# Kernel tuning notes

Measured on AMD Instinct MI355X. Metric: run time of the kernel, lower is better.

The kernel has to match this reference:

```python
import jax, jax.numpy as jnp
import numpy as np

N, E = 50000, 800000
IN_DIM, H, D = 128, 8, 16  # num_heads=8, out_dim(per head)=16


def setup_inputs() -> dict:
    key = jax.random.key(0)
    ks = jax.random.split(key, 9)
    s = 1.0 / np.sqrt(IN_DIM)
    return {
        "h": jax.random.normal(ks[0], (N, IN_DIM), dtype=jnp.float32),
        "Wq": jax.random.normal(ks[1], (IN_DIM, H * D), dtype=jnp.float32) * s,
        "bq": jnp.zeros((H * D,), dtype=jnp.float32),
        "Wk": jax.random.normal(ks[2], (IN_DIM, H * D), dtype=jnp.float32) * s,
        "bk": jnp.zeros((H * D,), dtype=jnp.float32),
        "Wv": jax.random.normal(ks[3], (IN_DIM, H * D), dtype=jnp.float32) * s,
        "bv": jnp.zeros((H * D,), dtype=jnp.float32),
        "src": jax.random.randint(ks[4], (E,), 0, N, dtype=jnp.int32),
        "dst": jax.random.randint(ks[5], (E,), 0, N, dtype=jnp.int32),
    }


def reference(h, Wq, bq, Wk, bk, Wv, bv, src, dst):
    n = h.shape[0]
    Q = (h @ Wq + bq).reshape(n, H, D)
    K = (h @ Wk + bk).reshape(n, H, D)
    V = (h @ Wv + bv).reshape(n, H, D)
    # edge score: u_mul_v(K, Q).sum(-1) / sqrt(D), clamped to [-5, 5]
    score = jnp.einsum("ehd,ehd->eh", K[src], Q[dst]) / jnp.sqrt(
        jnp.asarray(D, h.dtype)
    )  # [E, H]
    score = jnp.clip(score, -5.0, 5.0)
    # edge_softmax over edges sharing the same destination node
    smax = jax.ops.segment_max(score, dst, num_segments=n)  # [N, H]
    ex = jnp.exp(score - smax[dst])
    denom = jax.ops.segment_sum(ex, dst, num_segments=n)  # [N, H]
    a = ex / denom[dst]  # [E, H]
    # u_mul_e(V, a) then sum to destination
    m = V[src] * a[:, :, None]  # [E, H, D]
    wV = jax.ops.segment_sum(m, dst, num_segments=n)  # [N, H, D]
    return wV.reshape(n, H * D)
```

## Files before the change

kernel.cpp:

```cpp
#include <hip/hip_runtime.h>
#include <hip/hip_bf16.h>


typedef short short8 __attribute__((ext_vector_type(8)));
typedef float f32x4 __attribute__((ext_vector_type(4)));

__device__ __forceinline__ unsigned pack_bf16(float a, float b) {
    unsigned ua = __float_as_uint(a), ub = __float_as_uint(b);
    ua += 0x7fffu + ((ua >> 16) & 1u);
    ub += 0x7fffu + ((ub >> 16) & 1u);
    return (ua >> 16) | (ub & 0xffff0000u);
}

#define ULO(u) __uint_as_float((u) << 16)
#define UHI(u) __uint_as_float((u) & 0xffff0000u)

__global__ __launch_bounds__(256) void prep_all(
    const float* __restrict__ W0, const float* __restrict__ W1,
    const float* __restrict__ W2, unsigned char* __restrict__ WTb,
    int* __restrict__ counts, int n)
{
    const int b = blockIdx.x;
    if (b < 24) {
        const int w   = b >> 3;
        const int idx = (b & 7) * 256 + threadIdx.x;
        const float* W = (w == 0) ? W0 : (w == 1) ? W1 : W2;
        unsigned char* wt = WTb + w * 32768;
        const int kp = idx >> 5;
        const int c4 = (idx & 31) * 4;
        const float* Wp = W + (size_t)(2 * kp) * 128 + c4;
        float4 wa = *(const float4*)Wp;
        float4 wb = *(const float4*)(Wp + 128);
        float a0[4] = {wa.x, wa.y, wa.z, wa.w};
        float a1[4] = {wb.x, wb.y, wb.z, wb.w};
#pragma unroll
        for (int i = 0; i < 4; ++i) {
            const int col = c4 + i;
            *(unsigned*)(wt + col * 256 + ((4 * kp) ^ ((col & 7) << 4))) =
                pack_bf16(a0[i], a1[i]);
        }
    } else {
        const int i = (b - 24) * 256 + threadIdx.x;
        if (i < n) counts[i] = 0;
    }
}

__global__ void hist_rank(const int* __restrict__ dst, int* __restrict__ counts,
                          int* __restrict__ rank, int e) {
    int i = blockIdx.x * blockDim.x + threadIdx.x;
    if (i < e) rank[i] = atomicAdd(&counts[dst[i]], 1);
}

__global__ void scan_block_sums(const int* __restrict__ counts, int* __restrict__ bsums, int nelem) {
    __shared__ int red[4];
    int i = blockIdx.x * 256 + threadIdx.x;
    int v = (i < nelem) ? counts[i] : 0;
#pragma unroll
    for (int o = 32; o > 0; o >>= 1) v += __shfl_down(v, o, 64);
    if ((threadIdx.x & 63) == 0) red[threadIdx.x >> 6] = v;
    __syncthreads();
    if (threadIdx.x == 0) bsums[blockIdx.x] = red[0] + red[1] + red[2] + red[3];
}

__global__ void scan_final2(const int* __restrict__ counts, const int* __restrict__ bsums,
                            int* __restrict__ offsets, int nelem, int e) {
    __shared__ int tmp[256];
    __shared__ int red[4];
    const int t = threadIdx.x;

    int pre = (t < blockIdx.x) ? bsums[t] : 0;
#pragma unroll
    for (int o = 32; o > 0; o >>= 1) pre += __shfl_down(pre, o, 64);
    if ((t & 63) == 0) red[t >> 6] = pre;
    __syncthreads();
    const int base = red[0] + red[1] + red[2] + red[3];

    const int i = blockIdx.x * 256 + t;
    int v = (i < nelem) ? counts[i] : 0;
    tmp[t] = v;
    __syncthreads();
    for (int o = 1; o < 256; o <<= 1) {
        int u = (t >= o) ? tmp[t - o] : 0;
        __syncthreads();
        tmp[t] += u;
        __syncthreads();
    }
    if (i < nelem) offsets[i] = base + tmp[t] - v;
    if (i == nelem) offsets[nelem] = e;
}

__global__ void fill_kernel(const int* __restrict__ src, const int* __restrict__ dst,
                            const int* __restrict__ rank, const int* __restrict__ offsets,
                            int* __restrict__ srcSorted, int e) {
    int i = blockIdx.x * blockDim.x + threadIdx.x;
    if (i < e) srcSorted[offsets[dst[i]] + rank[i]] = src[i];
}

__global__ __launch_bounds__(512) void qkv_gemm(
    const float* __restrict__ h, const unsigned char* __restrict__ WTb,
    const float* __restrict__ b0, const float* __restrict__ b1,
    const float* __restrict__ b2,
    unsigned* __restrict__ qb, unsigned* __restrict__ kb, unsigned* __restrict__ vb,
    int n)
{
    __shared__ __align__(16) unsigned char lds[32768];
    const int tid  = threadIdx.x;
    const int row0 = blockIdx.x * 64;

    for (int idx = tid; idx < 2048; idx += 512) {
        const int row = idx >> 5;
        const int c4  = (idx & 31) * 4;
        float4 v = make_float4(0.f, 0.f, 0.f, 0.f);
        if (row0 + row < n) v = *(const float4*)(h + (size_t)(row0 + row) * 128 + c4);
        *(uint2*)(lds + row * 256 + ((c4 * 2) ^ ((row & 7) << 4))) =
            make_uint2(pack_bf16(v.x, v.y), pack_bf16(v.z, v.w));
    }

    const float* bs[3] = {b0, b1, b2};
    unsigned* planes[3] = {qb, kb, vb};

    const int lane = tid & 63, wave = tid >> 6;
    const int wr = wave >> 2, wc = wave & 3;
    const int lr = lane & 15, lg = lane >> 4;

    __syncthreads();

    short8 af[2][4];
#pragma unroll
    for (int mt = 0; mt < 2; ++mt)
#pragma unroll
        for (int ks = 0; ks < 4; ++ks) {
            const int row = wr * 32 + mt * 16 + lr;
            const int kbyte = ks * 64 + lg * 16;
            af[mt][ks] = *(const short8*)(lds + row * 256 + (kbyte ^ ((row & 7) << 4)));
        }

    for (int w = 0; w < 3; ++w) {
        short8 bf[2][4];
#pragma unroll
        for (int nt = 0; nt < 2; ++nt)
#pragma unroll
            for (int ks = 0; ks < 4; ++ks) {
                const int col = wc * 32 + nt * 16 + lr;
                const int kbyte = ks * 64 + lg * 16;
                bf[nt][ks] = *(const short8*)(
                    WTb + w * 32768 + col * 256 + (kbyte ^ ((col & 7) << 4)));
            }

        f32x4 acc[2][2];
#pragma unroll
        for (int nt = 0; nt < 2; ++nt) {
            const float bv = bs[w][wc * 32 + nt * 16 + lr];
            acc[0][nt] = (f32x4){bv, bv, bv, bv};
            acc[1][nt] = (f32x4){bv, bv, bv, bv};
        }
#pragma unroll
        for (int ks = 0; ks < 4; ++ks)
#pragma unroll
            for (int mt = 0; mt < 2; ++mt)
#pragma unroll
                for (int nt = 0; nt < 2; ++nt)
                    acc[mt][nt] = __builtin_amdgcn_mfma_f32_16x16x32_bf16(
                        af[mt][ks], bf[nt][ks], acc[mt][nt], 0, 0, 0);

        __syncthreads();
        {
            unsigned* epi = (unsigned*)(lds + 16384);
#pragma unroll
            for (int mt = 0; mt < 2; ++mt)
#pragma unroll
                for (int nt = 0; nt < 2; ++nt) {
                    const int col = wc * 32 + nt * 16 + lr;
#pragma unroll
                    for (int r = 0; r < 4; ++r) {
                        const int row = wr * 32 + mt * 16 + lg * 4 + r;
                        const float v  = acc[mt][nt][r];
                        const float vn = __shfl_xor(v, 1);
                        if (!(lane & 1)) epi[row * 64 + (col >> 1)] = pack_bf16(v, vn);
                    }
                }
        }
        __syncthreads();
        {
            const uint4* s = (const uint4*)(lds + 16384);
            uint4* d = (uint4*)(planes[w] + (size_t)row0 * 64);
            d[tid]       = s[tid];
            d[tid + 512] = s[tid + 512];
        }
    }
}

__global__ __launch_bounds__(256) void mha_node(
    const unsigned* __restrict__ Qb, const unsigned* __restrict__ Kb,
    const unsigned* __restrict__ Vb,
    const int* __restrict__ offsets, const int* __restrict__ srcSorted,
    float* __restrict__ out, int n)
{
    const int lane = threadIdx.x & 63;
    const int node = (blockIdx.x * blockDim.x + threadIdx.x) >> 6;
    if (node >= n) return;

    const unsigned qu = Qb[(size_t)node * 64 + lane];
    const float qx = ULO(qu) * 0.25f, qy = UHI(qu) * 0.25f;
    const int beg = offsets[node], end = offsets[node + 1];

    float accx = 0.f, accy = 0.f, lsum = 0.f;

#define EDGE_COMPUTE(ku, vu)                                          \
    {                                                                 \
        float prod = fmaf(ULO(ku), qx, UHI(ku) * qy);                 \
        prod += __shfl_xor(prod, 1);                                  \
        prod += __shfl_xor(prod, 2);                                  \
        prod += __shfl_xor(prod, 4);                                  \
        float sc = fminf(5.f, fmaxf(-5.f, prod));                     \
        float p = __expf(sc);                                         \
        lsum += p;                                                    \
        accx = fmaf(p, ULO(vu), accx);                                \
        accy = fmaf(p, UHI(vu), accy);                                \
    }

    for (int j0 = beg; j0 < end; j0 += 64) {
        const int rem = end - j0;
        const int cnt = rem < 64 ? rem : 64;
        int myS = (lane < cnt) ? srcSorted[j0 + lane] : 0;

        int t = 0;
        for (; t + 8 <= cnt; t += 8) {
            unsigned ku[8], vu[8];
#pragma unroll
            for (int u = 0; u < 8; ++u) {
                int s = __shfl(myS, t + u);
                ku[u] = Kb[(size_t)s * 64 + lane];
                vu[u] = Vb[(size_t)s * 64 + lane];
            }
#pragma unroll
            for (int u = 0; u < 8; ++u) EDGE_COMPUTE(ku[u], vu[u]);
        }
        for (; t < cnt; ++t) {
            int s = __shfl(myS, t);
            unsigned ku0 = Kb[(size_t)s * 64 + lane];
            unsigned vu0 = Vb[(size_t)s * 64 + lane];
            EDGE_COMPUTE(ku0, vu0);
        }
    }

    float inv = (lsum > 0.f) ? 1.f / lsum : 0.f;
    *(float2*)(out + (size_t)node * 128 + lane * 2) =
        make_float2(accx * inv, accy * inv);
}

extern "C" void kernel_launch(void* const* d_in, const int* in_sizes, int n_in,
                              void* d_out, int out_size, void* d_ws, size_t ws_size,
                              hipStream_t stream) {
    const float* h  = (const float*)d_in[0];
    const float* Wq = (const float*)d_in[1];
    const float* bq = (const float*)d_in[2];
    const float* Wk = (const float*)d_in[3];
    const float* bk = (const float*)d_in[4];
    const float* Wv = (const float*)d_in[5];
    const float* bv = (const float*)d_in[6];
    const int*   src = (const int*)d_in[7];
    const int*   dst = (const int*)d_in[8];
    float* out = (float*)d_out;

    const int n = in_sizes[0] / 128;
    const int e = in_sizes[7];
    const int nblk = (n + 63) / 64;
    const int npad = nblk * 64;
    const int nb = (n + 255) / 256;

    char* ws = (char*)d_ws;
    size_t off = 0;
    auto alloc = [&](size_t bytes) {
        char* p = ws + off;
        off = (off + bytes + 255) & ~(size_t)255;
        return p;
    };
    unsigned char* WTb = (unsigned char*)alloc(3 * 32768);
    unsigned* Qb       = (unsigned*)alloc((size_t)npad * 64 * 4);
    unsigned* Kb       = (unsigned*)alloc((size_t)npad * 64 * 4);
    unsigned* Vb       = (unsigned*)alloc((size_t)npad * 64 * 4);
    int* counts        = (int*)alloc((size_t)n * sizeof(int));
    int* offsets       = (int*)alloc((size_t)(n + 1) * sizeof(int));
    int* rank          = (int*)alloc((size_t)e * sizeof(int));
    int* bsums         = (int*)alloc((size_t)nb * sizeof(int));
    int* srcSorted     = (int*)alloc((size_t)e * sizeof(int));
    (void)ws_size; (void)n_in; (void)out_size;

    prep_all<<<24 + nb, 256, 0, stream>>>(Wq, Wk, Wv, WTb, counts, n);
    hist_rank<<<(e + 255) / 256, 256, 0, stream>>>(dst, counts, rank, e);
    scan_block_sums<<<nb, 256, 0, stream>>>(counts, bsums, n);
    scan_final2<<<nb, 256, 0, stream>>>(counts, bsums, offsets, n, e);
    fill_kernel<<<(e + 255) / 256, 256, 0, stream>>>(src, dst, rank, offsets, srcSorted, e);
    qkv_gemm<<<nblk, 512, 0, stream>>>(h, WTb, bq, bk, bv, Qb, Kb, Vb, n);
    mha_node<<<((size_t)n * 64 + 255) / 256, 256, 0, stream>>>(
        Qb, Kb, Vb, offsets, srcSorted, out, n);
}
```

Before: 143.7 us.

## Interleave K and V per node and compute transposed GEMM without LDS

K and V projections are now written into one interleaved buffer, so each edge gather in the attention kernel fetches K and V with a single 8-byte load per lane instead of two separate 4-byte loads from different planes. The QKV GEMM is transposed: weights become the A operand and h rows are loaded straight from global into registers as the B operand. This removes the LDS staging, the swizzle, and the block barriers. Outputs are written directly from the accumulators, which makes the stores less coalesced (scattered 4-byte writes for K and V) in exchange for better gather locality in the dominant edge loop.

After: 162.6 us. +13.2%, slower.

```diff
diff --git a/kernel.cpp b/kernel.cpp
--- a/kernel.cpp
+++ b/kernel.cpp
@@ -36,8 +36,7 @@
 #pragma unroll
         for (int i = 0; i < 4; ++i) {
             const int col = c4 + i;
-            *(unsigned*)(wt + col * 256 + ((4 * kp) ^ ((col & 7) << 4))) =
-                pack_bf16(a0[i], a1[i]);
+            *(unsigned*)(wt + col * 256 + kp * 4) = pack_bf16(a0[i], a1[i]);
         }
     } else {
         const int i = (b - 24) * 256 + threadIdx.x;
@@ -96,64 +95,56 @@
     if (i < e) srcSorted[offsets[dst[i]] + rank[i]] = src[i];
 }
 
-__global__ __launch_bounds__(512) void qkv_gemm(
+__global__ __launch_bounds__(512) void qkv_gemm_t(
     const float* __restrict__ h, const unsigned char* __restrict__ WTb,
     const float* __restrict__ b0, const float* __restrict__ b1,
     const float* __restrict__ b2,
-    unsigned* __restrict__ qb, unsigned* __restrict__ kb, unsigned* __restrict__ vb,
-    int n)
+    unsigned* __restrict__ qb, unsigned* __restrict__ kvb, int n)
 {
-    __shared__ __align__(16) unsigned char lds[32768];
     const int tid  = threadIdx.x;
+    const int lane = tid & 63, wave = tid >> 6;
+    const int a = wave >> 2;
+    const int bq4 = wave & 3;
+    const int lr = lane & 15, lg = lane >> 4;
     const int row0 = blockIdx.x * 64;
 
-    for (int idx = tid; idx < 2048; idx += 512) {
-        const int row = idx >> 5;
-        const int c4  = (idx & 31) * 4;
-        float4 v = make_float4(0.f, 0.f, 0.f, 0.f);
-        if (row0 + row < n) v = *(const float4*)(h + (size_t)(row0 + row) * 128 + c4);
-        *(uint2*)(lds + row * 256 + ((c4 * 2) ^ ((row & 7) << 4))) =
-            make_uint2(pack_bf16(v.x, v.y), pack_bf16(v.z, v.w));
+    short8 hf[2][4];
+#pragma unroll
+    for (int nt = 0; nt < 2; ++nt) {
+        const int node = row0 + a * 32 + nt * 16 + lr;
+        const bool ok = node < n;
+        const float* hp = h + (size_t)node * 128;
+#pragma unroll
+        for (int ks = 0; ks < 4; ++ks) {
+            const int k0 = ks * 32 + lg * 8;
+            float4 x = ok ? *(const float4*)(hp + k0)     : make_float4(0.f,0.f,0.f,0.f);
+            float4 y = ok ? *(const float4*)(hp + k0 + 4) : make_float4(0.f,0.f,0.f,0.f);
+            uint4 u = make_uint4(pack_bf16(x.x, x.y), pack_bf16(x.z, x.w),
+                                 pack_bf16(y.x, y.y), pack_bf16(y.z, y.w));
+            hf[nt][ks] = *(short8*)&u;
+        }
     }
 
     const float* bs[3] = {b0, b1, b2};
-    unsigned* planes[3] = {qb, kb, vb};
-
-    const int lane = tid & 63, wave = tid >> 6;
-    const int wr = wave >> 2, wc = wave & 3;
-    const int lr = lane & 15, lg = lane >> 4;
-
-    __syncthreads();
-
-    short8 af[2][4];
-#pragma unroll
-    for (int mt = 0; mt < 2; ++mt)
-#pragma unroll
-        for (int ks = 0; ks < 4; ++ks) {
-            const int row = wr * 32 + mt * 16 + lr;
-            const int kbyte = ks * 64 + lg * 16;
-            af[mt][ks] = *(const short8*)(lds + row * 256 + (kbyte ^ ((row & 7) << 4)));
-        }
 
     for (int w = 0; w < 3; ++w) {
-        short8 bf[2][4];
-#pragma unroll
-        for (int nt = 0; nt < 2; ++nt)
-#pragma unroll
-            for (int ks = 0; ks < 4; ++ks) {
-                const int col = wc * 32 + nt * 16 + lr;
-                const int kbyte = ks * 64 + lg * 16;
-                bf[nt][ks] = *(const short8*)(
-                    WTb + w * 32768 + col * 256 + (kbyte ^ ((col & 7) << 4)));
-            }
+        short8 af[2][4];
+#pragma unroll
+        for (int mt = 0; mt < 2; ++mt) {
+            const unsigned char* wp = WTb + w * 32768 + (bq4 * 32 + mt * 16 + lr) * 256;
+#pragma unroll
+            for (int ks = 0; ks < 4; ++ks)
+                af[mt][ks] = *(const short8*)(wp + ks * 64 + lg * 16);
+        }
 
         f32x4 acc[2][2];
 #pragma unroll
-        for (int nt = 0; nt < 2; ++nt) {
-            const float bv = bs[w][wc * 32 + nt * 16 + lr];
-            acc[0][nt] = (f32x4){bv, bv, bv, bv};
-            acc[1][nt] = (f32x4){bv, bv, bv, bv};
-        }
+        for (int mt = 0; mt < 2; ++mt) {
+            const float4 bv = *(const float4*)(bs[w] + bq4 * 32 + mt * 16 + lg * 4);
+            acc[mt][0] = (f32x4){bv.x, bv.y, bv.z, bv.w};
+            acc[mt][1] = acc[mt][0];
+        }
+
 #pragma unroll
         for (int ks = 0; ks < 4; ++ks)
 #pragma unroll
@@ -161,38 +152,32 @@
 #pragma unroll
                 for (int nt = 0; nt < 2; ++nt)
                     acc[mt][nt] = __builtin_amdgcn_mfma_f32_16x16x32_bf16(
-                        af[mt][ks], bf[nt][ks], acc[mt][nt], 0, 0, 0);
-
-        __syncthreads();
-        {
-            unsigned* epi = (unsigned*)(lds + 16384);
-#pragma unroll
-            for (int mt = 0; mt < 2; ++mt)
-#pragma unroll
-                for (int nt = 0; nt < 2; ++nt) {
-                    const int col = wc * 32 + nt * 16 + lr;
-#pragma unroll
-                    for (int r = 0; r < 4; ++r) {
-                        const int row = wr * 32 + mt * 16 + lg * 4 + r;
-                        const float v  = acc[mt][nt][r];
-                        const float vn = __shfl_xor(v, 1);
-                        if (!(lane & 1)) epi[row * 64 + (col >> 1)] = pack_bf16(v, vn);
-                    }
+                        af[mt][ks], hf[nt][ks], acc[mt][nt], 0, 0, 0);
+
+#pragma unroll
+        for (int mt = 0; mt < 2; ++mt) {
+            const int pi = bq4 * 16 + mt * 8 + lg * 2;
+#pragma unroll
+            for (int nt = 0; nt < 2; ++nt) {
+                const int node = row0 + a * 32 + nt * 16 + lr;
+                const unsigned u0 = pack_bf16(acc[mt][nt][0], acc[mt][nt][1]);
+                const unsigned u1 = pack_bf16(acc[mt][nt][2], acc[mt][nt][3]);
+                if (w == 0) {
+                    *(uint2*)(qb + (size_t)node * 64 + pi) = make_uint2(u0, u1);
+                } else if (w == 1) {
+                    kvb[(size_t)node * 128 + 2 * pi]     = u0;
+                    kvb[(size_t)node * 128 + 2 * pi + 2] = u1;
+                } else {
+                    kvb[(size_t)node * 128 + 2 * pi + 1] = u0;
+                    kvb[(size_t)node * 128 + 2 * pi + 3] = u1;
                 }
-        }
-        __syncthreads();
-        {
-            const uint4* s = (const uint4*)(lds + 16384);
-            uint4* d = (uint4*)(planes[w] + (size_t)row0 * 64);
-            d[tid]       = s[tid];
-            d[tid + 512] = s[tid + 512];
+            }
         }
     }
 }
 
 __global__ __launch_bounds__(256) void mha_node(
-    const unsigned* __restrict__ Qb, const unsigned* __restrict__ Kb,
-    const unsigned* __restrict__ Vb,
+    const unsigned* __restrict__ Qb, const uint2* __restrict__ KV,
     const int* __restrict__ offsets, const int* __restrict__ srcSorted,
     float* __restrict__ out, int n)
 {
@@ -206,17 +191,17 @@
 
     float accx = 0.f, accy = 0.f, lsum = 0.f;
 
-#define EDGE_COMPUTE(ku, vu)                                          \
+#define EDGE_COMPUTE(kv)                                              \
     {                                                                 \
-        float prod = fmaf(ULO(ku), qx, UHI(ku) * qy);                 \
+        float prod = fmaf(ULO((kv).x), qx, UHI((kv).x) * qy);         \
         prod += __shfl_xor(prod, 1);                                  \
         prod += __shfl_xor(prod, 2);                                  \
         prod += __shfl_xor(prod, 4);                                  \
         float sc = fminf(5.f, fmaxf(-5.f, prod));                     \
         float p = __expf(sc);                                         \
         lsum += p;                                                    \
-        accx = fmaf(p, ULO(vu), accx);                                \
-        accy = fmaf(p, UHI(vu), accy);                                \
+        accx = fmaf(p, ULO((kv).y), accx);                            \
+        accy = fmaf(p, UHI((kv).y), accy);                            \
     }
 
     for (int j0 = beg; j0 < end; j0 += 64) {
@@ -226,21 +211,19 @@
 
         int t = 0;
         for (; t + 8 <= cnt; t += 8) {
-            unsigned ku[8], vu[8];
+            uint2 kv[8];
 #pragma unroll
             for (int u = 0; u < 8; ++u) {
                 int s = __shfl(myS, t + u);
-                ku[u] = Kb[(size_t)s * 64 + lane];
-                vu[u] = Vb[(size_t)s * 64 + lane];
+                kv[u] = KV[(size_t)s * 64 + lane];
             }
 #pragma unroll
-            for (int u = 0; u < 8; ++u) EDGE_COMPUTE(ku[u], vu[u]);
+            for (int u = 0; u < 8; ++u) EDGE_COMPUTE(kv[u]);
         }
         for (; t < cnt; ++t) {
             int s = __shfl(myS, t);
-            unsigned ku0 = Kb[(size_t)s * 64 + lane];
-            unsigned vu0 = Vb[(size_t)s * 64 + lane];
-            EDGE_COMPUTE(ku0, vu0);
+            uint2 kv0 = KV[(size_t)s * 64 + lane];
+            EDGE_COMPUTE(kv0);
         }
     }
 
@@ -278,8 +261,7 @@
     };
     unsigned char* WTb = (unsigned char*)alloc(3 * 32768);
     unsigned* Qb       = (unsigned*)alloc((size_t)npad * 64 * 4);
-    unsigned* Kb       = (unsigned*)alloc((size_t)npad * 64 * 4);
-    unsigned* Vb       = (unsigned*)alloc((size_t)npad * 64 * 4);
+    unsigned* KVb      = (unsigned*)alloc((size_t)npad * 128 * 4);
     int* counts        = (int*)alloc((size_t)n * sizeof(int));
     int* offsets       = (int*)alloc((size_t)(n + 1) * sizeof(int));
     int* rank          = (int*)alloc((size_t)e * sizeof(int));
@@ -292,7 +274,7 @@
     scan_block_sums<<<nb, 256, 0, stream>>>(counts, bsums, n);
     scan_final2<<<nb, 256, 0, stream>>>(counts, bsums, offsets, n, e);
     fill_kernel<<<(e + 255) / 256, 256, 0, stream>>>(src, dst, rank, offsets, srcSorted, e);
-    qkv_gemm<<<nblk, 512, 0, stream>>>(h, WTb, bq, bk, bv, Qb, Kb, Vb, n);
+    qkv_gemm_t<<<nblk, 512, 0, stream>>>(h, WTb, bq, bk, bv, Qb, KVb, n);
     mha_node<<<((size_t)n * 64 + 255) / 256, 256, 0, stream>>>(
-        Qb, Kb, Vb, offsets, srcSorted, out, n);
-}
+        Qb, (const uint2*)KVb, offsets, srcSorted, out, n);
+}
```

## Interleave K/V into one buffer and process two edges per wave in mha_node

Applied to the files above, without the earlier changes.

Stores K and V interleaved per node so each lane fetches K and V features with a single 16-byte load. Each half-wave processes a different edge, with a cross-half reduction at the end. This halves the load instruction count for edge gathers and improves coalescing. It also fuses the histogram into the weight-prep kernel, replaces the zeroing with a memset, and drops the weight swizzle. The GEMM epilogue now stages K and V in LDS to write the interleaved layout, using more shared memory.

Result: slower. 154.3 us (+7.4%).

```diff
diff --git a/kernel.cpp b/kernel.cpp
--- a/kernel.cpp
+++ b/kernel.cpp
@@ -15,10 +15,11 @@
 #define ULO(u) __uint_as_float((u) << 16)
 #define UHI(u) __uint_as_float((u) & 0xffff0000u)
 
-__global__ __launch_bounds__(256) void prep_all(
+__global__ __launch_bounds__(256) void prep_hist(
     const float* __restrict__ W0, const float* __restrict__ W1,
     const float* __restrict__ W2, unsigned char* __restrict__ WTb,
-    int* __restrict__ counts, int n)
+    const int* __restrict__ dst, int* __restrict__ counts,
+    int* __restrict__ rank, int e)
 {
     const int b = blockIdx.x;
     if (b < 24) {
@@ -34,21 +35,12 @@
         float a0[4] = {wa.x, wa.y, wa.z, wa.w};
         float a1[4] = {wb.x, wb.y, wb.z, wb.w};
 #pragma unroll
-        for (int i = 0; i < 4; ++i) {
-            const int col = c4 + i;
-            *(unsigned*)(wt + col * 256 + ((4 * kp) ^ ((col & 7) << 4))) =
-                pack_bf16(a0[i], a1[i]);
-        }
+        for (int i = 0; i < 4; ++i)
+            *(unsigned*)(wt + (c4 + i) * 256 + kp * 4) = pack_bf16(a0[i], a1[i]);
     } else {
         const int i = (b - 24) * 256 + threadIdx.x;
-        if (i < n) counts[i] = 0;
-    }
-}
-
-__global__ void hist_rank(const int* __restrict__ dst, int* __restrict__ counts,
-                          int* __restrict__ rank, int e) {
-    int i = blockIdx.x * blockDim.x + threadIdx.x;
-    if (i < e) rank[i] = atomicAdd(&counts[dst[i]], 1);
+        if (i < e) rank[i] = atomicAdd(&counts[dst[i]], 1);
+    }
 }
 
 __global__ void scan_block_sums(const int* __restrict__ counts, int* __restrict__ bsums, int nelem) {
@@ -100,10 +92,9 @@
     const float* __restrict__ h, const unsigned char* __restrict__ WTb,
     const float* __restrict__ b0, const float* __restrict__ b1,
     const float* __restrict__ b2,
-    unsigned* __restrict__ qb, unsigned* __restrict__ kb, unsigned* __restrict__ vb,
-    int n)
+    unsigned* __restrict__ qb, unsigned* __restrict__ kvb, int n)
 {
-    __shared__ __align__(16) unsigned char lds[32768];
+    __shared__ __align__(16) unsigned char lds[49152];
     const int tid  = threadIdx.x;
     const int row0 = blockIdx.x * 64;
 
@@ -117,8 +108,6 @@
     }
 
     const float* bs[3] = {b0, b1, b2};
-    unsigned* planes[3] = {qb, kb, vb};
-
     const int lane = tid & 63, wave = tid >> 6;
     const int wr = wave >> 2, wc = wave & 3;
     const int lr = lane & 15, lg = lane >> 4;
@@ -135,6 +124,9 @@
             af[mt][ks] = *(const short8*)(lds + row * 256 + (kbyte ^ ((row & 7) << 4)));
         }
 
+    unsigned* epiA = (unsigned*)(lds + 16384);
+    unsigned* epiB = (unsigned*)(lds + 32768);
+
     for (int w = 0; w < 3; ++w) {
         short8 bf[2][4];
 #pragma unroll
@@ -142,9 +134,8 @@
 #pragma unroll
             for (int ks = 0; ks < 4; ++ks) {
                 const int col = wc * 32 + nt * 16 + lr;
-                const int kbyte = ks * 64 + lg * 16;
                 bf[nt][ks] = *(const short8*)(
-                    WTb + w * 32768 + col * 256 + (kbyte ^ ((col & 7) << 4)));
+                    WTb + w * 32768 + col * 256 + ks * 64 + lg * 16);
             }
 
         f32x4 acc[2][2];
@@ -165,7 +156,7 @@
 
         __syncthreads();
         {
-            unsigned* epi = (unsigned*)(lds + 16384);
+            unsigned* epi = (w == 2) ? epiB : epiA;
 #pragma unroll
             for (int mt = 0; mt < 2; ++mt)
 #pragma unroll
@@ -180,43 +171,57 @@
                     }
                 }
         }
-        __syncthreads();
-        {
-            const uint4* s = (const uint4*)(lds + 16384);
-            uint4* d = (uint4*)(planes[w] + (size_t)row0 * 64);
+        if (w == 0) {
+            __syncthreads();
+            const uint4* s = (const uint4*)epiA;
+            uint4* d = (uint4*)(qb + (size_t)row0 * 64);
             d[tid]       = s[tid];
             d[tid + 512] = s[tid + 512];
+        } else if (w == 2) {
+            __syncthreads();
+            for (int idx = tid; idx < 2048; idx += 512) {
+                const int row = idx >> 5, c = idx & 31;
+                uint4 o = make_uint4(epiA[row * 64 + 2 * c], epiA[row * 64 + 2 * c + 1],
+                                     epiB[row * 64 + 2 * c], epiB[row * 64 + 2 * c + 1]);
+                *(uint4*)(kvb + (size_t)(row0 + row) * 128 + c * 4) = o;
+            }
         }
     }
 }
 
 __global__ __launch_bounds__(256) void mha_node(
-    const unsigned* __restrict__ Qb, const unsigned* __restrict__ Kb,
-    const unsigned* __restrict__ Vb,
+    const unsigned* __restrict__ Qb, const uint4* __restrict__ KV4,
     const int* __restrict__ offsets, const int* __restrict__ srcSorted,
     float* __restrict__ out, int n)
 {
     const int lane = threadIdx.x & 63;
     const int node = (blockIdx.x * blockDim.x + threadIdx.x) >> 6;
     if (node >= n) return;
-
-    const unsigned qu = Qb[(size_t)node * 64 + lane];
-    const float qx = ULO(qu) * 0.25f, qy = UHI(qu) * 0.25f;
+    const int half = lane >> 5;
+    const int l5   = lane & 31;
+
+    const uint2 qu = *(const uint2*)(Qb + (size_t)node * 64 + 2 * l5);
+    const float q0 = ULO(qu.x) * 0.25f, q1 = UHI(qu.x) * 0.25f;
+    const float q2 = ULO(qu.y) * 0.25f, q3 = UHI(qu.y) * 0.25f;
+
     const int beg = offsets[node], end = offsets[node + 1];
-
-    float accx = 0.f, accy = 0.f, lsum = 0.f;
-
-#define EDGE_COMPUTE(ku, vu)                                          \
-    {                                                                 \
-        float prod = fmaf(ULO(ku), qx, UHI(ku) * qy);                 \
-        prod += __shfl_xor(prod, 1);                                  \
-        prod += __shfl_xor(prod, 2);                                  \
-        prod += __shfl_xor(prod, 4);                                  \
-        float sc = fminf(5.f, fmaxf(-5.f, prod));                     \
-        float p = __expf(sc);                                         \
-        lsum += p;                                                    \
-        accx = fmaf(p, ULO(vu), accx);                                \
-        accy = fmaf(p, UHI(vu), accy);                                \
+    float a0 = 0.f, a1 = 0.f, a2 = 0.f, a3 = 0.f, lsum = 0.f;
+
+#define PAIR_COMPUTE(kv, val)                                           \
+    {                                                                   \
+        float prod = ULO((kv).x) * q0;                                  \
+        prod = fmaf(UHI((kv).x), q1, prod);                             \
+        prod = fmaf(ULO((kv).y), q2, prod);                             \
+        prod = fmaf(UHI((kv).y), q3, prod);                             \
+        prod += __shfl_xor(prod, 1);                                    \
+        prod += __shfl_xor(prod, 2);                                    \
+        float sc = fminf(5.f, fmaxf(-5.f, prod));                       \
+        float p = (val) ? __expf(sc) : 0.f;                             \
+        lsum += p;                                                      \
+        a0 = fmaf(p, ULO((kv).z), a0);                                  \
+        a1 = fmaf(p, UHI((kv).z), a1);                                  \
+        a2 = fmaf(p, ULO((kv).w), a2);                                  \
+        a3 = fmaf(p, UHI((kv).w), a3);                                  \
     }
 
     for (int j0 = beg; j0 < end; j0 += 64) {
@@ -226,27 +231,35 @@
 
         int t = 0;
         for (; t + 8 <= cnt; t += 8) {
-            unsigned ku[8], vu[8];
-#pragma unroll
-            for (int u = 0; u < 8; ++u) {
-                int s = __shfl(myS, t + u);
-                ku[u] = Kb[(size_t)s * 64 + lane];
-                vu[u] = Vb[(size_t)s * 64 + lane];
+            uint4 kv[4];
+#pragma unroll
+            for (int u = 0; u < 4; ++u) {
+                int s = __shfl(myS, t + 2 * u + half);
+                kv[u] = KV4[(size_t)s * 32 + l5];
             }
 #pragma unroll
-            for (int u = 0; u < 8; ++u) EDGE_COMPUTE(ku[u], vu[u]);
-        }
-        for (; t < cnt; ++t) {
-            int s = __shfl(myS, t);
-            unsigned ku0 = Kb[(size_t)s * 64 + lane];
-            unsigned vu0 = Vb[(size_t)s * 64 + lane];
-            EDGE_COMPUTE(ku0, vu0);
-        }
-    }
-
-    float inv = (lsum > 0.f) ? 1.f / lsum : 0.f;
-    *(float2*)(out + (size_t)node * 128 + lane * 2) =
-        make_float2(accx * inv, accy * inv);
+            for (int u = 0; u < 4; ++u) PAIR_COMPUTE(kv[u], true);
+        }
+        for (; t < cnt; t += 2) {
+            const int ei = t + half;
+            const bool val = ei < cnt;
+            int s = __shfl(myS, val ? ei : cnt - 1);
+            uint4 kv0 = KV4[(size_t)s * 32 + l5];
+            PAIR_COMPUTE(kv0, val);
+        }
+    }
+
+    lsum += __shfl_xor(lsum, 32);
+    a0 += __shfl_xor(a0, 32);
+    a1 += __shfl_xor(a1, 32);
+    a2 += __shfl_xor(a2, 32);
+    a3 += __shfl_xor(a3, 32);
+
+    if (half == 0) {
+        const float inv = (lsum > 0.f) ? 1.f / lsum : 0.f;
+        *(float4*)(out + (size_t)node * 128 + 4 * l5) =
+            make_float4(a0 * inv, a1 * inv, a2 * inv, a3 * inv);
+    }
 }
 
 extern "C" void kernel_launch(void* const* d_in, const int* in_sizes, int n_in,
@@ -268,6 +281,7 @@
     const int nblk = (n + 63) / 64;
     const int npad = nblk * 64;
     const int nb = (n + 255) / 256;
+    const int eB = (e + 255) / 256;
 
     char* ws = (char*)d_ws;
     size_t off = 0;
@@ -278,8 +292,7 @@
     };
     unsigned char* WTb = (unsigned char*)alloc(3 * 32768);
     unsigned* Qb       = (unsigned*)alloc((size_t)npad * 64 * 4);
-    unsigned* Kb       = (unsigned*)alloc((size_t)npad * 64 * 4);
-    unsigned* Vb       = (unsigned*)alloc((size_t)npad * 64 * 4);
+    unsigned* KVb      = (unsigned*)alloc((size_t)npad * 128 * 4);
     int* counts        = (int*)alloc((size_t)n * sizeof(int));
     int* offsets       = (int*)alloc((size_t)(n + 1) * sizeof(int));
     int* rank          = (int*)alloc((size_t)e * sizeof(int));
@@ -287,12 +300,12 @@
     int* srcSorted     = (int*)alloc((size_t)e * sizeof(int));
     (void)ws_size; (void)n_in; (void)out_size;
 
-    prep_all<<<24 + nb, 256, 0, stream>>>(Wq, Wk, Wv, WTb, counts, n);
-    hist_rank<<<(e + 255) / 256, 256, 0, stream>>>(dst, counts, rank, e);
+    hipMemsetAsync(counts, 0, (size_t)n * sizeof(int), stream);
+    prep_hist<<<24 + eB, 256, 0, stream>>>(Wq, Wk, Wv, WTb, dst, counts, rank, e);
     scan_block_sums<<<nb, 256, 0, stream>>>(counts, bsums, n);
     scan_final2<<<nb, 256, 0, stream>>>(counts, bsums, offsets, n, e);
-    fill_kernel<<<(e + 255) / 256, 256, 0, stream>>>(src, dst, rank, offsets, srcSorted, e);
-    qkv_gemm<<<nblk, 512, 0, stream>>>(h, WTb, bq, bk, bv, Qb, Kb, Vb, n);
+    fill_kernel<<<eB, 256, 0, stream>>>(src, dst, rank, offsets, srcSorted, e);
+    qkv_gemm<<<nblk, 512, 0, stream>>>(h, WTb, bq, bk, bv, Qb, KVb, n);
     mha_node<<<((size_t)n * 64 + 255) / 256, 256, 0, stream>>>(
-        Qb, Kb, Vb, offsets, srcSorted, out, n);
-}
+        Qb, (const uint4*)KVb, offsets, srcSorted, out, n);
+}
```
